# Optimization experiments

Measured on AMD Instinct MI355X. Metric: run time of the kernel, lower is better.

## Reference

```python
import jax, jax.numpy as jnp
import numpy as np

CH = 192; NH = 8; HD = CH // NH; WS = 8; OV = 2; WSO = WS + 2 * OV
SCALE = HD ** -0.5
B, H, W = 2, 256, 256

# static relative-position index (matches WindowMSA._idx)
_gy, _gx = np.meshgrid(np.arange(WS), np.arange(WS), indexing='ij')
_flat = np.stack([_gy.ravel(), _gx.ravel()])            # [2, ws*ws]
_rel = _flat[:, :, None] - _flat[:, None, :]
_rel[0] += WS - 1; _rel[1] += WS - 1; _rel[0] *= 2 * WS - 1
RPE_IDX = jnp.asarray(_rel.sum(0), dtype=jnp.int32)     # [64, 64]


def _ln(x, g, b, eps=1e-5):
    m = jnp.mean(x, -1, keepdims=True)
    v = jnp.mean((x - m) ** 2, -1, keepdims=True)
    return (x - m) * jax.lax.rsqrt(v + eps) * g + b


def _partition(xhw):  # [B,H,W,C] -> [B*nw, ws*ws, C]
    b, h, w, c = xhw.shape
    x = xhw.reshape(b, h // WS, WS, w // WS, WS, c).transpose(0, 1, 3, 2, 4, 5)
    return x.reshape(-1, WS * WS, c)


def _reverse(xw, h, w, b):  # [B*nw, ws*ws, C] -> [B,H,W,C]
    c = xw.shape[-1]
    x = xw.reshape(b, h // WS, w // WS, WS, WS, c).transpose(0, 1, 3, 2, 4, 5)
    return x.reshape(b, h, w, c)


def _mha(q, k, v, bias=None):  # q:[n,Nq,C] k,v:[n,Nk,C] split into heads
    n, nq, c = q.shape
    nk = k.shape[1]
    q = q.reshape(n, nq, NH, HD).transpose(0, 2, 1, 3)
    k = k.reshape(n, nk, NH, HD).transpose(0, 2, 1, 3)
    v = v.reshape(n, nk, NH, HD).transpose(0, 2, 1, 3)
    attn = jnp.einsum('bhnd,bhmd->bhnm', q, k) * SCALE
    if bias is not None:
        attn = attn + bias
    attn = jax.nn.softmax(attn, axis=-1)
    out = jnp.einsum('bhnm,bhmd->bhnd', attn, v)
    return out.transpose(0, 2, 1, 3).reshape(n, nq, c)


def _forward(x, g1, b1, qkv_w, rpe, wproj_w, g2, b2, mlp_w1, mlp_w2,
             alpha, og, ob, q_w, kv_w, oproj_w):
    b, c, h, w = x.shape  # H,W are multiples of WS -> no window padding
    xhw = x.transpose(0, 2, 3, 1)  # BHWC

    # --- window MSA branch (shift=False) ---
    xw = _partition(xhw)  # [b*nw, 64, C]
    xn = _ln(xw, g1, b1)
    qkv = xn @ qkv_w.T  # [n, 64, 3C]
    q, k, v = jnp.split(qkv, 3, axis=-1)
    bias = rpe[RPE_IDX].transpose(2, 0, 1)[None]  # [1, nh, 64, 64]
    msa = _mha(q, k, v, bias) @ wproj_w.T
    xw = xw + msa
    hmid = _ln(xw, g2, b2) @ mlp_w1.T
    xw = xw + jax.nn.gelu(hmid, approximate=False) @ mlp_w2.T
    x_win = _reverse(xw, h, w, b).transpose(0, 3, 1, 2)  # BCHW

    # --- overlapping cross attention branch ---
    xwin = _partition(xhw)  # queries from non-overlapped windows [n, 64, C]
    q = _ln(xwin, og, ob) @ q_w.T
    xp2 = jnp.pad(x, ((0, 0), (0, 0), (OV, OV), (OV, OV)), mode='reflect')
    xp2 = xp2.transpose(0, 2, 3, 1)  # [B, H+2ov, W+2ov, C]
    nh_w, nw_w = h // WS, w // WS
    rows = (jnp.arange(nh_w) * WS)[:, None] + jnp.arange(WSO)[None, :]
    cols = (jnp.arange(nw_w) * WS)[:, None] + jnp.arange(WSO)[None, :]
    xuf = xp2[:, rows]            # [B, nh_w, wso, W+2ov, C]
    xuf = xuf[:, :, :, cols]      # [B, nh_w, wso, nw_w, wso, C]
    xuf = xuf.transpose(0, 1, 3, 2, 4, 5).reshape(-1, WSO * WSO, c)
    kv = xuf @ kv_w.T             # [n, 144, 2C]
    k, v = jnp.split(kv, 2, axis=-1)
    out = _mha(q, k, v) @ oproj_w.T + xwin
    x_oca = _reverse(out, h, w, b).transpose(0, 3, 1, 2)

    return x + x_win * alpha + x_oca * (1.0 - alpha)


def setup_inputs():
    key = jax.random.key(0)
    ks = jax.random.split(key, 10)
    f = lambda k, shape: jax.random.normal(k, shape, jnp.float32) * 0.02
    return {
        'x': jax.random.normal(ks[0], (B, CH, H, W), jnp.float32),
        'g1': jnp.ones((CH,), jnp.float32), 'b1': jnp.zeros((CH,), jnp.float32),
        'qkv_w': f(ks[1], (3 * CH, CH)),
        'rpe': f(ks[2], ((2 * WS - 1) ** 2, NH)),
        'wproj_w': f(ks[3], (CH, CH)),
        'g2': jnp.ones((CH,), jnp.float32), 'b2': jnp.zeros((CH,), jnp.float32),
        'mlp_w1': f(ks[4], (2 * CH, CH)), 'mlp_w2': f(ks[5], (CH, 2 * CH)),
        'alpha': jnp.float32(0.5),
        'og': jnp.ones((CH,), jnp.float32), 'ob': jnp.zeros((CH,), jnp.float32),
        'q_w': f(ks[6], (CH, CH)), 'kv_w': f(ks[7], (2 * CH, CH)),
        'oproj_w': f(ks[8], (CH, CH)),
    }


def reference(x, g1, b1, qkv_w, rpe, wproj_w, g2, b2, mlp_w1, mlp_w2,
              alpha, og, ob, q_w, kv_w, oproj_w):
    return _forward(x, g1, b1, qkv_w, rpe, wproj_w, g2, b2, mlp_w1, mlp_w2,
                    alpha, og, ob, q_w, kv_w, oproj_w)
```

## Files before the change

kernel.cpp:

```cpp
#include <hip/hip_runtime.h>
#include <hip/hip_bf16.h>

typedef unsigned short u16;
typedef unsigned int   u32;
typedef __attribute__((ext_vector_type(8))) short bf16x8;
typedef __attribute__((ext_vector_type(4))) float f32x4;

#define CH   192
#define NH   8
#define HWD  256
#define LDW  200
#define QSTR 28
#define SCALE 0.20412414523193154f

__device__ __forceinline__ float bf2f(u16 u){ u32 v = ((u32)u) << 16; return __builtin_bit_cast(float, v); }
__device__ __forceinline__ u16 f2bf(float f){
  u32 u = __builtin_bit_cast(u32, f);
  u = (u + 0x7fffu + ((u >> 16) & 1u)) >> 16;
  return (u16)u;
}
__device__ __forceinline__ float lo2f(u32 p){ return __builtin_bit_cast(float, p << 16); }
__device__ __forceinline__ float hi2f(u32 p){ return __builtin_bit_cast(float, p & 0xffff0000u); }
__device__ __forceinline__ void up8(uint4 q, float* f){
  f[0]=lo2f(q.x); f[1]=hi2f(q.x); f[2]=lo2f(q.y); f[3]=hi2f(q.y);
// ... 61 lines not shown
  for (int e = 0; e < 8; ++e){
    float w = s[e];
    if (gv) w *= gv[kb + e];
    d[e] = f2bf(w);
  }
}
__global__ void k_cvec(const float* __restrict__ W, const float* __restrict__ g,
                       const float* __restrict__ b, float* __restrict__ c1,
                       float* __restrict__ c2, int K){
  int n = blockIdx.x; int l = threadIdx.x;
  float s1 = 0.f, s2 = 0.f;
  for (int k = l; k < K; k += 64){
    float w = W[(size_t)n*K + k];
    s1 += w*g[k]; s2 += w*b[k];
  }
  #pragma unroll
  for (int d = 1; d < 64; d <<= 1){ s1 += __shfl_xor(s1, d, 64); s2 += __shfl_xor(s2, d, 64); }
  if (l == 0){ c1[n] = s1; c2[n] = s2; }
}

__global__ __launch_bounds__(512) void k_kv(const float* __restrict__ x,
                                            const u16* __restrict__ wkv,
                                            u16* __restrict__ KV){
  __shared__ __align__(16) u16 sA[64*LDW];
  const int blk = blockIdx.x;
  const int batch = blk >> 10;
  const int pix0 = (blk & 1023) * 64;
  const float* xb = x + (size_t)batch*CH*65536;

  for (int idx = threadIdx.x; idx < 1536; idx += 512){
    int c = idx >> 3, s = idx & 7;
    const float* p = xb + (size_t)c*65536 + pix0 + s*8;
    float4 a = *reinterpret_cast<const float4*>(p);
    float4 b = *reinterpret_cast<const float4*>(p + 4);
    u16* d = &sA[(s*8)*LDW + c];
    d[0*LDW]=f2bf(a.x); d[1*LDW]=f2bf(a.y); d[2*LDW]=f2bf(a.z); d[3*LDW]=f2bf(a.w);
    d[4*LDW]=f2bf(b.x); d[5*LDW]=f2bf(b.y); d[6*LDW]=f2bf(b.z); d[7*LDW]=f2bf(b.w);
  }
  __syncthreads();

  const int w = threadIdx.x >> 6, l = threadIdx.x & 63;
  const int mt = w >> 1, half = w & 1;
  const f32x4 z4 = {0.f,0.f,0.f,0.f};
  f32x4 acc[12];
  #pragma unroll
  for (int j = 0; j < 12; ++j) acc[j] = z4;
  const int arow = mt*16 + (l & 15);
  for (int kt = 0; kt < 6; ++kt){
    bf16x8 a = afrag(sA, 0, LDW, arow, kt, l);
    #pragma unroll
    for (int j = 0; j < 12; ++j){
      int nt = half*12 + j;
      acc[j] = mfma16(a, bfrag(wkv, nt*6 + kt, l), acc[j]);
    }
  }
  u16* kvb = KV + ((size_t)batch*65536 + pix0)*384;
  const int rbase = mt*16 + ((l>>4)<<2);
  #pragma unroll
  for (int j = 0; j < 12; ++j){
    int col = (half*12 + j)*16 + (l & 15);
    #pragma unroll
    for (int r = 0; r < 4; ++r)
      kvb[(size_t)(rbase + r)*384 + col] = f2bf(acc[j][r]);
  }
}

#define P_   0
#define OW_  0
#define XO_  0
#define OQ_  12800
#define KF_  25600
#define VT_  30208
#define STM_ 35584
#define STS_ 35840
#define OST_ 36096
#define OPOOLN 36352

template<int MODE>
__global__ __launch_bounds__(512) void k_oca_attn(
    const float* __restrict__ x, const u16* __restrict__ ws16, const float* __restrict__ wsf,
    const float* __restrict__ alpha_p, float* __restrict__ out, u16* __restrict__ xoca)
{
  __shared__ __align__(16) u16 pool[OPOOLN];
  float* stm = reinterpret_cast<float*>(pool + STM_);
  float* sts = reinterpret_cast<float*>(pool + STS_);
  float* st  = reinterpret_cast<float*>(pool + OST_);
  const u16* KV = ws16 + WS_KV/2;
  const u16* WQ = ws16 + WS_WQ/2;
  const u16* WO = ws16 + WS_WO/2;
  const float* c1o = wsf + WS_C1O/4;
  const float* c2o = wsf + WS_C2O/4;

  const int tid = threadIdx.x;
  const int win = blockIdx.x;
  const int b  = win >> 10;
  const int wy = (win >> 5) & 31;
  const int wx = win & 31;
  const int hrow = wy*8, wcol = wx*8;
  const float* xb = x + (size_t)b*CH*HWD*HWD;
  float* outb = out + (size_t)b*CH*HWD*HWD;
  const size_t pixBase = (size_t)b*65536;
  const f32x4 z4 = {0.f,0.f,0.f,0.f};

  for (int j = tid; j < 1536; j += 512){
    int c = j >> 3, ty = j & 7;
    const float* src = xb + ((size_t)c*HWD + hrow + ty)*HWD + wcol;
    float4 a = *reinterpret_cast<const float4*>(src);
    float4 q = *reinterpret_cast<const float4*>(src + 4);
    u16* dst = &pool[OW_ + (ty*8)*LDW + c];
    dst[0*LDW]=f2bf(a.x); dst[1*LDW]=f2bf(a.y); dst[2*LDW]=f2bf(a.z); dst[3*LDW]=f2bf(a.w);
    dst[4*LDW]=f2bf(q.x); dst[5*LDW]=f2bf(q.y); dst[6*LDW]=f2bf(q.z); dst[7*LDW]=f2bf(q.w);
  }
  __syncthreads();
  ln_stats(pool + OW_, st, tid);
  __syncthreads();

  const int w = tid >> 6, l = tid & 63;
  const int mt = w >> 1;
  const int arow = mt*16 + (l & 15);
  const int rbase = mt*16 + ((l>>4)<<2);

  {
    const int half = w & 1;
    f32x4 acc[6];
    #pragma unroll
    for (int j = 0; j < 6; ++j) acc[j] = z4;
    for (int kt = 0; kt < 6; ++kt){
      bf16x8 a = afrag(pool, OW_, LDW, arow, kt, l);
      #pragma unroll
      for (int j = 0; j < 6; ++j)
        acc[j] = mfma16(a, bfrag(WQ, (half*6 + j)*6 + kt, l), acc[j]);
    }
    float mr[4], rr[4];
    #pragma unroll
    for (int r = 0; r < 4; ++r){ mr[r] = st[(rbase+r)*2]; rr[r] = st[(rbase+r)*2+1]; }
    #pragma unroll
    for (int j = 0; j < 6; ++j){
      int col = (half*6 + j)*16 + (l & 15);
      float c1v = c1o[col], c2v = c2o[col];
      #pragma unroll
      for (int r = 0; r < 4; ++r)
        pool[OQ_ + (rbase + r)*LDW + col] = f2bf(SCALE*(rr[r]*(acc[j][r] - mr[r]*c1v) + c2v));
    }
  }
  __syncthreads();

  {
    const uint4 zz = make_uint4(0,0,0,0);
    for (int i = tid; i < 64; i += 512)
      *reinterpret_cast<uint4*>(pool + OQ_ + i*LDW + 192) = zz;
    for (int i = tid; i < 144; i += 512)
      *reinterpret_cast<uint4*>(pool + KF_ + (i>>4)*512 + 384 + (i&15)*8) = zz;
    for (int i = tid; i < 672; i += 512)
      *reinterpret_cast<uint4*>(pool + VT_ + i*8) = zz;
    for (int i = tid; i < 128; i += 512)
      *reinterpret_cast<uint4*>(pool + P_ + (i>>1)*168 + 144 + (i&1)*8) = zz;
  }
  __syncthreads();

  const int ng   = w & 1;
  const int ntlo = ng ? 4 : 0;
  const int ntn  = ng ? 5 : 4;

  for (int h = 0; h < NH; ++h){
    for (int i = tid; i < 432; i += 512){
      int tok = i / 3, seg = i - tok*3;
      int ti = tok / 12, tj = tok - ti*12;
      int pix = refl(hrow + ti - 2)*HWD + refl(wcol + tj - 2);
      const u16* src = KV + (pixBase + (size_t)pix)*384 + h*24 + seg*8;
      uint4 kk = *reinterpret_cast<const uint4*>(src);
      uint4 vv = *reinterpret_cast<const uint4*>(src + 192);
      *reinterpret_cast<uint4*>(pool + KF_ + (tok>>4)*512 + (seg*16 + (tok&15))*8) = kk;
      const u16* vp = reinterpret_cast<const u16*>(&vv);
      #pragma unroll
      for (int e = 0; e < 8; ++e)
        pool[VT_ + (seg*8 + e)*168 + tok] = vp[e];
    }
    __syncthreads();

    f32x4 S[5];
    #pragma unroll
    for (int t = 0; t < 5; ++t) S[t] = z4;
    {
      bf16x8 a = *reinterpret_cast<const bf16x8*>(pool + OQ_ + arow*LDW + h*24 + ((l>>4)<<3));
      #pragma unroll
      for (int t = 0; t < 5; ++t)
        if (t < ntn)
          S[t] = mfma16(a, *reinterpret_cast<const bf16x8*>(pool + KF_ + (ntlo + t)*512 + l*8), z4);
    }
    #pragma unroll
    for (int r = 0; r < 4; ++r){
      float mx = -3.0e38f;
      #pragma unroll
      for (int t = 0; t < 5; ++t) if (t < ntn) mx = fmaxf(mx, S[t][r]);
      mx = fmaxf(mx, __shfl_xor(mx, 1, 64));
      mx = fmaxf(mx, __shfl_xor(mx, 2, 64));
      mx = fmaxf(mx, __shfl_xor(mx, 4, 64));
      mx = fmaxf(mx, __shfl_xor(mx, 8, 64));
      if ((l & 15) == 0) stm[(rbase + r)*2 + ng] = mx;
    }
    __syncthreads();

    #pragma unroll
    for (int r = 0; r < 4; ++r){
      int row = rbase + r;
      float m = fmaxf(stm[row*2], stm[row*2 + 1]);
      float sum = 0.f;
      #pragma unroll
      for (int t = 0; t < 5; ++t) if (t < ntn){
        float p = __expf(S[t][r] - m);
        sum += p;
        pool[P_ + row*168 + (ntlo + t)*16 + (l & 15)] = f2bf(p);
      }
      sum += __shfl_xor(sum, 1, 64);
      sum += __shfl_xor(sum, 2, 64);
      sum += __shfl_xor(sum, 4, 64);
      sum += __shfl_xor(sum, 8, 64);
      if ((l & 15) == 0) sts[row*2 + ng] = sum;
    }
    __syncthreads();

    {
      f32x4 O = z4;
      #pragma unroll
      for (int kt = 0; kt < 5; ++kt){
        bf16x8 pa = *reinterpret_cast<const bf16x8*>(pool + P_  + arow*168 + kt*32 + ((l>>4)<<3));
        bf16x8 vb = *reinterpret_cast<const bf16x8*>(pool + VT_ + (ng*16 + (l & 15))*168 + kt*32 + ((l>>4)<<3));
        O = mfma16(pa, vb, O);
      }
      int d = ng*16 + (l & 15);
      if (d < 24){
        #pragma unroll
        for (int r = 0; r < 4; ++r){
          int row = rbase + r;
          float inv = 1.f / (sts[row*2] + sts[row*2 + 1]);
          pool[OQ_ + row*LDW + h*24 + d] = f2bf(O[r]*inv);
        }
      }
    }
    __syncthreads();
  }

  {
    const int half = w & 1;
    f32x4 acc[6];
    #pragma unroll
    for (int j = 0; j < 6; ++j) acc[j] = z4;
    for (int kt = 0; kt < 6; ++kt){
      bf16x8 a = afrag(pool, OQ_, LDW, arow, kt, l);
      #pragma unroll
      for (int j = 0; j < 6; ++j)
        acc[j] = mfma16(a, bfrag(WO, (half*6 + j)*6 + kt, l), acc[j]);
    }
    __syncthreads();
    #pragma unroll
    for (int j = 0; j < 6; ++j){
      int col = (half*6 + j)*16 + (l & 15);
      #pragma unroll
      for (int r = 0; r < 4; ++r)
        pool[XO_ + (rbase + r)*LDW + col] = f2bf(acc[j][r]);
    }
  }
  __syncthreads();

  if (MODE == 0){
    float beta = 1.f - alpha_p[0];
    float xg = 1.f + beta;
    for (int j = tid; j < 1536; j += 512){
      int c = j >> 3, ty = j & 7;
      size_t goff = ((size_t)c*HWD + hrow + ty)*HWD + wcol;
      const float* src = xb + goff;
      float4 a = *reinterpret_cast<const float4*>(src);
      float4 q = *reinterpret_cast<const float4*>(src + 4);
      float wv[8];
      #pragma unroll
      for (int e = 0; e < 8; ++e) wv[e] = bf2f(pool[XO_ + (ty*8 + e)*LDW + c]);
      float4 o1 = make_float4(xg*a.x + beta*wv[0], xg*a.y + beta*wv[1], xg*a.z + beta*wv[2], xg*a.w + beta*wv[3]);
      float4 o2 = make_float4(xg*q.x + beta*wv[4], xg*q.y + beta*wv[5], xg*q.z + beta*wv[6], xg*q.w + beta*wv[7]);
      *reinterpret_cast<float4*>(outb + goff)     = o1;
      *reinterpret_cast<float4*>(outb + goff + 4) = o2;
    }
  } else {
    u16* xw = xoca + (size_t)win*12288;
    for (int j = tid; j < 1536; j += 512){
      int c = j >> 3, ty = j & 7;
      size_t goff = ((size_t)c*HWD + hrow + ty)*HWD + wcol;
      const float* src = xb + goff;
      float4 a = *reinterpret_cast<const float4*>(src);
      float4 q = *reinterpret_cast<const float4*>(src + 4);
      float xv[8] = {a.x,a.y,a.z,a.w,q.x,q.y,q.z,q.w};
      u32 wds[4];
      #pragma unroll
      for (int e = 0; e < 4; ++e){
        u32 lo = f2bf(bf2f(pool[XO_ + (ty*8 + 2*e  )*LDW + c]) + xv[2*e]);
        u32 hi = f2bf(bf2f(pool[XO_ + (ty*8 + 2*e+1)*LDW + c]) + xv[2*e+1]);
        wds[e] = lo | (hi << 16);
      }
      uint4 o; o.x = wds[0]; o.y = wds[1]; o.z = wds[2]; o.w = wds[3];
      *reinterpret_cast<uint4*>(xw + c*64 + ty*8) = o;
    }
  }
}

#define SX   0
#define SN   12800
#define SQKV 25600
#define SG   25600
#define SM   62464
#define SST  75264
#define POOLSZ 75520

template<int MODE>
__global__ __launch_bounds__(512) void k_msa(
    const float* __restrict__ x, const u16* __restrict__ ws16, const float* __restrict__ wsf,
    const float* __restrict__ rpe, const float* __restrict__ alpha_p, float* __restrict__ out,
    const u16* __restrict__ xoca)
{
  __shared__ __align__(16) u16 pool[POOLSZ];
  float* st = reinterpret_cast<float*>(pool + SST);
  const u16* W1  = ws16 + WS_W1/2;
  const u16* WP  = ws16 + WS_WP/2;
  const u16* WM1 = ws16 + WS_WM1/2;
  const u16* WM2 = ws16 + WS_WM2/2;
  const float* c1  = wsf + WS_C1/4;
  const float* c2  = wsf + WS_C2/4;
  const float* c1m = wsf + WS_C1M/4;
  const float* c2m = wsf + WS_C2M/4;

  const int tid = threadIdx.x;
  const int win = blockIdx.x;
  const int b  = win >> 10;
  const int wy = (win >> 5) & 31;
  const int wx = win & 31;
  const int hrow = wy*8, wcol = wx*8;
  const float* xb = x + (size_t)b*CH*HWD*HWD;
  float* outb = out + (size_t)b*CH*HWD*HWD;

  for (int j = tid; j < 1536; j += 512){
    int c = j >> 3, ty = j & 7;
    const float* src = xb + ((size_t)c*HWD + hrow + ty)*HWD + wcol;
    float4 a = *reinterpret_cast<const float4*>(src);
    float4 q = *reinterpret_cast<const float4*>(src + 4);
    u16* dst = &pool[SX + (ty*8)*LDW + c];
    dst[0*LDW]=f2bf(a.x); dst[1*LDW]=f2bf(a.y); dst[2*LDW]=f2bf(a.z); dst[3*LDW]=f2bf(a.w);
    dst[4*LDW]=f2bf(q.x); dst[5*LDW]=f2bf(q.y); dst[6*LDW]=f2bf(q.z); dst[7*LDW]=f2bf(q.w);
  }
  __syncthreads();
  ln_stats(pool + SX, st, tid);
  __syncthreads();

  const int w = tid >> 6, l = tid & 63;
  const int mt = w >> 1, half = w & 1;
  const int arow = mt*16 + (l & 15);
  const int rbase = mt*16 + ((l>>4)<<2);
  const f32x4 z4 = {0.f,0.f,0.f,0.f};

  {
    f32x4 acc[18];
    #pragma unroll
    for (int j = 0; j < 18; ++j) acc[j] = z4;
    for (int kt = 0; kt < 6; ++kt){
      bf16x8 a = afrag(pool, SX, LDW, arow, kt, l);
      #pragma unroll
      for (int j = 0; j < 18; ++j)
        acc[j] = mfma16(a, bfrag(W1, (half*18 + j)*6 + kt, l), acc[j]);
    }
    float mr[4], rr[4];
    #pragma unroll
    for (int r = 0; r < 4; ++r){ mr[r] = st[(rbase+r)*2]; rr[r] = st[(rbase+r)*2+1]; }
    #pragma unroll
    for (int j = 0; j < 18; ++j){
      int col = (half*18 + j)*16 + (l & 15);
      float c1v = c1[col], c2v = c2[col];
      #pragma unroll
      for (int r = 0; r < 4; ++r){
        int row = rbase + r;
        float v = rr[r]*(acc[j][r] - mr[r]*c1v) + c2v;
        pool[SQKV + row*576 + (col ^ (((row>>3)&7)<<3))] = f2bf(v);
      }
    }
  }
  __syncthreads();

  {
    const int t8 = tid >> 3, s8 = tid & 7;
    const int ry = t8 >> 3, rx = t8 & 7;
    const int swq = ((t8 >> 3) & 7) << 3;
    const int swk = s8 << 3;
    for (int h = 0; h < NH; ++h){
      float p[8];
      {
        float q24[24];
        #pragma unroll
        for (int seg = 0; seg < 3; ++seg){
          uint4 v = *reinterpret_cast<const uint4*>(pool + SQKV + t8*576 + ((h*24 + seg*8) ^ swq));
          up8(v, q24 + seg*8);
        }
        #pragma unroll
        for (int j = 0; j < 8; ++j){
          int c = s8*8 + j;
          float k24[24];
          #pragma unroll
          for (int seg = 0; seg < 3; ++seg){
            uint4 v = *reinterpret_cast<const uint4*>(pool + SQKV + c*576 + ((192 + h*24 + seg*8) ^ swk));
            up8(v, k24 + seg*8);
          }
          float s = 0.f;
          #pragma unroll
          for (int e = 0; e < 24; ++e) s += q24[e]*k24[e];
          int cy = c >> 3, cx = c & 7;
          p[j] = s*SCALE + rpe[((ry-cy+7)*15 + (rx-cx+7))*NH + h];
        }
      }
      float mx = p[0];
      #pragma unroll
      for (int j = 1; j < 8; ++j) mx = fmaxf(mx, p[j]);
      mx = fmaxf(mx, __shfl_xor(mx, 1, 64));
      mx = fmaxf(mx, __shfl_xor(mx, 2, 64));
      mx = fmaxf(mx, __shfl_xor(mx, 4, 64));
      float sum = 0.f;
      #pragma unroll
      for (int j = 0; j < 8; ++j){ p[j] = __expf(p[j] - mx); sum += p[j]; }
      sum += __shfl_xor(sum, 1, 64); sum += __shfl_xor(sum, 2, 64); sum += __shfl_xor(sum, 4, 64);
      float inv = 1.f / sum;
      float o24[24];
      #pragma unroll
      for (int seg = 0; seg < 3; ++seg){
        float o8[8];
        #pragma unroll
        for (int e = 0; e < 8; ++e) o8[e] = 0.f;
        #pragma unroll
        for (int j = 0; j < 8; ++j){
          int c = s8*8 + j;
          uint4 v = *reinterpret_cast<const uint4*>(pool + SQKV + c*576 + ((384 + h*24 + seg*8) ^ swk));
          float v8[8]; up8(v, v8);
          #pragma unroll
          for (int e = 0; e < 8; ++e) o8[e] += p[j]*v8[e];
        }
        #pragma unroll
        for (int e = 0; e < 8; ++e) o24[seg*8 + e] = o8[e];
      }
      #pragma unroll
      for (int e = 0; e < 24; ++e){
        o24[e] += __shfl_xor(o24[e], 1, 64);
        o24[e] += __shfl_xor(o24[e], 2, 64);
        o24[e] += __shfl_xor(o24[e], 4, 64);
      }
      u16* mrow = &pool[SM + t8*LDW + h*24 + s8*3];
      #pragma unroll
      for (int o = 0; o < 3; ++o) mrow[o] = f2bf(o24[s8*3 + o]*inv);
    }
  }
  __syncthreads();

  {
    f32x4 acc[6];
    #pragma unroll
    for (int j = 0; j < 6; ++j) acc[j] = z4;
    for (int kt = 0; kt < 6; ++kt){
      bf16x8 a = afrag(pool, SM, LDW, arow, kt, l);
      #pragma unroll
      for (int j = 0; j < 6; ++j)
        acc[j] = mfma16(a, bfrag(WP, (half*6 + j)*6 + kt, l), acc[j]);
    }
    #pragma unroll
    for (int j = 0; j < 6; ++j){
      int col = (half*6 + j)*16 + (l & 15);
      #pragma unroll
      for (int r = 0; r < 4; ++r){
        int row = rbase + r;
        pool[SN + row*LDW + col] = f2bf(acc[j][r] + bf2f(pool[SX + row*LDW + col]));
      }
    }
  }
  __syncthreads();
  ln_stats(pool + SN, st, tid);
  __syncthreads();

  {
    f32x4 acc[12];
    #pragma unroll
    for (int j = 0; j < 12; ++j) acc[j] = z4;
    for (int kt = 0; kt < 6; ++kt){
      bf16x8 a = afrag(pool, SN, LDW, arow, kt, l);
      #pragma unroll
      for (int j = 0; j < 12; ++j)
        acc[j] = mfma16(a, bfrag(WM1, (half*12 + j)*6 + kt, l), acc[j]);
    }
    float mr[4], rr[4];
    #pragma unroll
    for (int r = 0; r < 4; ++r){ mr[r] = st[(rbase+r)*2]; rr[r] = st[(rbase+r)*2+1]; }
    #pragma unroll
    for (int j = 0; j < 12; ++j){
      int col = (half*12 + j)*16 + (l & 15);
      float c1v = c1m[col], c2v = c2m[col];
      #pragma unroll
      for (int r = 0; r < 4; ++r){
        float hv = rr[r]*(acc[j][r] - mr[r]*c1v) + c2v;
        float gl = 0.5f*hv*(1.f + erff(hv*0.70710678118654752f));
        pool[SG + (rbase + r)*392 + col] = f2bf(gl);
      }
    }
  }
  __syncthreads();

  {
    f32x4 acc[6];
    #pragma unroll
    for (int j = 0; j < 6; ++j) acc[j] = z4;
    for (int kt = 0; kt < 12; ++kt){
      bf16x8 a = afrag(pool, SG, 392, arow, kt, l);
      #pragma unroll
      for (int j = 0; j < 6; ++j)
        acc[j] = mfma16(a, bfrag(WM2, (half*6 + j)*12 + kt, l), acc[j]);
    }
    #pragma unroll
    for (int j = 0; j < 6; ++j){
      int col = (half*6 + j)*16 + (l & 15);
      #pragma unroll
      for (int r = 0; r < 4; ++r){
        int row = rbase + r;
        pool[SM + row*LDW + col] = f2bf(acc[j][r] + bf2f(pool[SN + row*LDW + col]));
      }
    }
  }
  __syncthreads();

  float alpha = alpha_p[0];
  if (MODE == 0){
    for (int j = tid; j < 1536; j += 512){
      int c = j >> 3, ty = j & 7;
      size_t goff = ((size_t)c*HWD + hrow + ty)*HWD + wcol;
      float* dst = outb + goff;
      float4 a = *reinterpret_cast<const float4*>(dst);
      float4 q = *reinterpret_cast<const float4*>(dst + 4);
      float wv[8];
      #pragma unroll
      for (int e = 0; e < 8; ++e) wv[e] = bf2f(pool[SM + (ty*8 + e)*LDW + c]);
      float4 o1 = make_float4(a.x + alpha*wv[0], a.y + alpha*wv[1], a.z + alpha*wv[2], a.w + alpha*wv[3]);
      float4 o2 = make_float4(q.x + alpha*wv[4], q.y + alpha*wv[5], q.z + alpha*wv[6], q.w + alpha*wv[7]);
      *reinterpret_cast<float4*>(dst)     = o1;
      *reinterpret_cast<float4*>(dst + 4) = o2;
    }
  } else {
    float beta = 1.f - alpha;
    const u16* xw = xoca + (size_t)win*12288;
    for (int j = tid; j < 1536; j += 512){
      int c = j >> 3, ty = j & 7;
      size_t goff = ((size_t)c*HWD + hrow + ty)*HWD + wcol;
      const float* src = xb + goff;
      float4 a = *reinterpret_cast<const float4*>(src);
      float4 q = *reinterpret_cast<const float4*>(src + 4);
      uint4 oc = *reinterpret_cast<const uint4*>(xw + c*64 + ty*8);
      float ov[8]; up8(oc, ov);
      float wv[8];
      #pragma unroll
      for (int e = 0; e < 8; ++e) wv[e] = bf2f(pool[SM + (ty*8 + e)*LDW + c]);
      float4 o1 = make_float4(a.x + alpha*wv[0] + beta*ov[0], a.y + alpha*wv[1] + beta*ov[1],
                              a.z + alpha*wv[2] + beta*ov[2], a.w + alpha*wv[3] + beta*ov[3]);
      float4 o2 = make_float4(q.x + alpha*wv[4] + beta*ov[4], q.y + alpha*wv[5] + beta*ov[5],
                              q.z + alpha*wv[6] + beta*ov[6], q.w + alpha*wv[7] + beta*ov[7]);
      *reinterpret_cast<float4*>(outb + goff)     = o1;
      *reinterpret_cast<float4*>(outb + goff + 4) = o2;
    }
  }
}

__device__ __forceinline__ void layernorm_fb(const u16* __restrict__ src, u16* __restrict__ dst,
                                             const float* __restrict__ g, const float* __restrict__ b,
                                             int tid)
{
  int r = tid >> 3, sub = tid & 7;
  const u16* row = src + r*LDW + sub*24;
  float v[24];
  float s = 0.f, s2 = 0.f;
  #pragma unroll
  for (int e = 0; e < 24; ++e){ v[e] = bf2f(row[e]); s += v[e]; s2 += v[e]*v[e]; }
  s  += __shfl_xor(s, 1, 64);  s  += __shfl_xor(s, 2, 64);  s  += __shfl_xor(s, 4, 64);
  s2 += __shfl_xor(s2, 1, 64); s2 += __shfl_xor(s2, 2, 64); s2 += __shfl_xor(s2, 4, 64);
  float m   = s * (1.f/192.f);
  float var = s2 * (1.f/192.f) - m*m;
  float rs  = rsqrtf(var + 1e-5f);
  u16* drow = dst + r*LDW + sub*24;
  #pragma unroll
  for (int e = 0; e < 24; ++e)
    drow[e] = f2bf((v[e] - m) * rs * g[sub*24+e] + b[sub*24+e]);
}
__device__ __forceinline__ void gemm83(const u16* __restrict__ a_lds,
                                       const float* __restrict__ w0,
                                       const float* __restrict__ w1,
                                       const float* __restrict__ w2,
                                       int tg, float (*acc)[3])
{
  for (int k0 = 0; k0 < 192; k0 += 8){
    float wv[3][8];
    ldw8(w0 + k0, wv[0]); ldw8(w1 + k0, wv[1]); ldw8(w2 + k0, wv[2]);
    #pragma unroll
    for (int tt = 0; tt < 8; ++tt){
      float a[8];
      up8(*reinterpret_cast<const uint4*>(a_lds + (tg*8+tt)*LDW + k0), a);
      #pragma unroll
      for (int e = 0; e < 8; ++e){
        acc[tt][0] += a[e]*wv[0][e];
        acc[tt][1] += a[e]*wv[1][e];
        acc[tt][2] += a[e]*wv[2][e];
      }
    }
  }
}
__global__ __launch_bounds__(512) void k_msa_fb(
    const float* __restrict__ x, const float* __restrict__ g1, const float* __restrict__ b1,
    const float* __restrict__ qkv_w, const float* __restrict__ rpe, const float* __restrict__ wproj,
    const float* __restrict__ g2, const float* __restrict__ b2,
    const float* __restrict__ mlp1, const float* __restrict__ mlp2,
    const float* __restrict__ alpha_p, float* __restrict__ out)
{
  __shared__ __align__(16) u16 sX[64*LDW];
  __shared__ __align__(16) u16 sN[64*LDW];
  __shared__ __align__(16) u16 sM[64*LDW];
  __shared__ __align__(16) float sQ[64*QSTR];
  __shared__ __align__(16) float sK[64*QSTR];
  __shared__ __align__(16) float sV[64*QSTR];
  const int tid = threadIdx.x;
  const int win = blockIdx.x;
  const int b  = win >> 10;
  const int wy = (win >> 5) & 31;
  const int wx = win & 31;
  const int hrow = wy*8, wcol = wx*8;
  const float* xb = x + (size_t)b*CH*HWD*HWD;
  float* outb = out + (size_t)b*CH*HWD*HWD;
  for (int j = tid; j < 1536; j += 512){
    int c = j >> 3, ty = j & 7;
    const float* src = xb + ((size_t)c*HWD + hrow + ty)*HWD + wcol;
    float4 a = *reinterpret_cast<const float4*>(src);
    float4 q = *reinterpret_cast<const float4*>(src + 4);
    u16* dst = &sX[(ty*8)*LDW + c];
    dst[0*LDW]=f2bf(a.x); dst[1*LDW]=f2bf(a.y); dst[2*LDW]=f2bf(a.z); dst[3*LDW]=f2bf(a.w);
    dst[4*LDW]=f2bf(q.x); dst[5*LDW]=f2bf(q.y); dst[6*LDW]=f2bf(q.z); dst[7*LDW]=f2bf(q.w);
  }
  __syncthreads();
  layernorm_fb(sX, sN, g1, b1, tid);
  __syncthreads();
  const int t8 = tid >> 3, s8 = tid & 7;
  for (int h = 0; h < NH; ++h){
    {
      const u16* arow = &sN[t8*LDW];
      float acc[9];
      #pragma unroll
      for (int o = 0; o < 9; ++o) acc[o] = 0.f;
      const float* wp[9];
      #pragma unroll
      for (int o = 0; o < 3; ++o){
        const float* base = qkv_w + (size_t)(h*24 + s8*3 + o)*192;
        wp[o] = base; wp[3+o] = base + 192*192; wp[6+o] = base + 2*192*192;
      }
      for (int k0 = 0; k0 < 192; k0 += 8){
        float a[8]; up8(*reinterpret_cast<const uint4*>(arow + k0), a);
        #pragma unroll
        for (int o = 0; o < 9; ++o){
          float wv[8]; ldw8(wp[o] + k0, wv);
          #pragma unroll
          for (int e = 0; e < 8; ++e) acc[o] += a[e]*wv[e];
        }
      }
      #pragma unroll
      for (int o = 0; o < 3; ++o){
        sQ[t8*QSTR + s8*3 + o] = acc[o];
        sK[t8*QSTR + s8*3 + o] = acc[3+o];
        sV[t8*QSTR + s8*3 + o] = acc[6+o];
      }
    }
    __syncthreads();
    {
      float q24[24];
      #pragma unroll
      for (int e = 0; e < 24; ++e) q24[e] = sQ[t8*QSTR + e];
      const int ry = t8 >> 3, rx = t8 & 7;
      float p[8];
      #pragma unroll
      for (int j = 0; j < 8; ++j){
        int c = s8*8 + j;
        const float* kr = &sK[c*QSTR];
        float s = 0.f;
        #pragma unroll
        for (int e = 0; e < 24; ++e) s += q24[e]*kr[e];
        int cy = c >> 3, cx = c & 7;
        p[j] = s*SCALE + rpe[((ry-cy+7)*15 + (rx-cx+7))*NH + h];
      }
      float mx = p[0];
      #pragma unroll
      for (int j = 1; j < 8; ++j) mx = fmaxf(mx, p[j]);
      mx = fmaxf(mx, __shfl_xor(mx, 1, 64));
      mx = fmaxf(mx, __shfl_xor(mx, 2, 64));
      mx = fmaxf(mx, __shfl_xor(mx, 4, 64));
      float sum = 0.f;
      #pragma unroll
      for (int j = 0; j < 8; ++j){ p[j] = __expf(p[j] - mx); sum += p[j]; }
      sum += __shfl_xor(sum, 1, 64); sum += __shfl_xor(sum, 2, 64); sum += __shfl_xor(sum, 4, 64);
      float inv = 1.f / sum;
      float o24[24];
      #pragma unroll
      for (int e = 0; e < 24; ++e) o24[e] = 0.f;
      #pragma unroll
      for (int j = 0; j < 8; ++j){
        const float* vr = &sV[(s8*8 + j)*QSTR];
        #pragma unroll
        for (int e = 0; e < 24; ++e) o24[e] += p[j]*vr[e];
      }
      #pragma unroll
      for (int e = 0; e < 24; ++e){
        o24[e] += __shfl_xor(o24[e], 1, 64);
        o24[e] += __shfl_xor(o24[e], 2, 64);
        o24[e] += __shfl_xor(o24[e], 4, 64);
      }
      u16* mrow = &sM[t8*LDW + h*24 + s8*3];
      #pragma unroll
      for (int o = 0; o < 3; ++o) mrow[o] = f2bf(o24[s8*3 + o]*inv);
    }
    __syncthreads();
  }
  const int tg = tid >> 6, cg = tid & 63;
  {
    float acc[8][3];
    #pragma unroll
    for (int tt = 0; tt < 8; ++tt){ acc[tt][0]=0.f; acc[tt][1]=0.f; acc[tt][2]=0.f; }
    gemm83(sM, wproj + (size_t)(cg*3+0)*192, wproj + (size_t)(cg*3+1)*192, wproj + (size_t)(cg*3+2)*192, tg, acc);
    #pragma unroll
    for (int tt = 0; tt < 8; ++tt)
      #pragma unroll
      for (int j = 0; j < 3; ++j){
        int t = tg*8+tt, c = cg*3+j;
        sN[t*LDW + c] = f2bf(acc[tt][j] + bf2f(sX[t*LDW + c]));
      }
  }
  __syncthreads();
  layernorm_fb(sN, sX, g2, b2, tid);
  __syncthreads();
  float facc[8][3];
  #pragma unroll
  for (int tt = 0; tt < 8; ++tt){ facc[tt][0]=0.f; facc[tt][1]=0.f; facc[tt][2]=0.f; }
  for (int half = 0; half < 2; ++half){
    {
      float acc[8][3];
      #pragma unroll
      for (int tt = 0; tt < 8; ++tt){ acc[tt][0]=0.f; acc[tt][1]=0.f; acc[tt][2]=0.f; }
      gemm83(sX, mlp1 + (size_t)(half*192 + cg*3+0)*192, mlp1 + (size_t)(half*192 + cg*3+1)*192,
                 mlp1 + (size_t)(half*192 + cg*3+2)*192, tg, acc);
      #pragma unroll
      for (int tt = 0; tt < 8; ++tt)
        #pragma unroll
        for (int j = 0; j < 3; ++j){
          float vv = acc[tt][j];
          sM[(tg*8+tt)*LDW + cg*3+j] = f2bf(0.5f*vv*(1.f + erff(vv*0.70710678118654752f)));
        }
    }
    __syncthreads();
    gemm83(sM, mlp2 + (size_t)(cg*3+0)*384 + half*192, mlp2 + (size_t)(cg*3+1)*384 + half*192,
               mlp2 + (size_t)(cg*3+2)*384 + half*192, tg, facc);
    __syncthreads();
  }
  #pragma unroll
  for (int tt = 0; tt < 8; ++tt)
    #pragma unroll
    for (int j = 0; j < 3; ++j){
      int t = tg*8+tt, c = cg*3+j;
      sM[t*LDW + c] = f2bf(bf2f(sN[t*LDW + c]) + facc[tt][j]);
    }
  __syncthreads();
  float alpha = alpha_p[0];
  for (int j = tid; j < 1536; j += 512){
    int c = j >> 3, ty = j & 7;
    size_t goff = ((size_t)c*HWD + hrow + ty)*HWD + wcol;
    const float* src = xb + goff;
    float4 a = *reinterpret_cast<const float4*>(src);
    float4 q = *reinterpret_cast<const float4*>(src + 4);
    float wv[8];
    #pragma unroll
    for (int e = 0; e < 8; ++e) wv[e] = bf2f(sM[(ty*8 + e)*LDW + c]);
    float4 o1 = make_float4(a.x + alpha*wv[0], a.y + alpha*wv[1], a.z + alpha*wv[2], a.w + alpha*wv[3]);
    float4 o2 = make_float4(q.x + alpha*wv[4], q.y + alpha*wv[5], q.z + alpha*wv[6], q.w + alpha*wv[7]);
    *reinterpret_cast<float4*>(outb + goff)     = o1;
    *reinterpret_cast<float4*>(outb + goff + 4) = o2;
  }
}
__global__ __launch_bounds__(512) void k_oca_fb(
    const float* __restrict__ x, const float* __restrict__ og_p, const float* __restrict__ ob_p,
    const float* __restrict__ q_w, const float* __restrict__ kv_w, const float* __restrict__ oproj,
    const float* __restrict__ alpha_p, float* __restrict__ out)
{
  __shared__ __align__(16) u16 sW[64*LDW];
  __shared__ __align__(16) u16 sN[64*LDW];
  __shared__ __align__(16) u16 sQa[64*LDW];
  __shared__ __align__(16) u16 sU[144*LDW];
  __shared__ __align__(16) u16 sKb[144*32];
  __shared__ __align__(16) u16 sVb[144*32];
  const int tid = threadIdx.x;
  const int win = blockIdx.x;
  const int b  = win >> 10;
  const int wy = (win >> 5) & 31;
  const int wx = win & 31;
  const int hrow = wy*8, wcol = wx*8;
  const float* xb = x + (size_t)b*CH*HWD*HWD;
  float* outb = out + (size_t)b*CH*HWD*HWD;
  for (int j = tid; j < 1536; j += 512){
    int c = j >> 3, ty = j & 7;
    const float* src = xb + ((size_t)c*HWD + hrow + ty)*HWD + wcol;
    float4 a = *reinterpret_cast<const float4*>(src);
    float4 q = *reinterpret_cast<const float4*>(src + 4);
    u16* dst = &sW[(ty*8)*LDW + c];
    dst[0*LDW]=f2bf(a.x); dst[1*LDW]=f2bf(a.y); dst[2*LDW]=f2bf(a.z); dst[3*LDW]=f2bf(a.w);
    dst[4*LDW]=f2bf(q.x); dst[5*LDW]=f2bf(q.y); dst[6*LDW]=f2bf(q.z); dst[7*LDW]=f2bf(q.w);
  }
  for (int i = tid; i < 144*192; i += 512){
    int c = i / 144, t = i - c*144;
    int ti = t / 12, tj = t - ti*12;
    sU[t*LDW + c] = f2bf(xb[((size_t)c*HWD + refl(hrow + ti - 2))*HWD + refl(wcol + tj - 2)]);
  }
  __syncthreads();
  layernorm_fb(sW, sN, og_p, ob_p, tid);
  __syncthreads();
  const int tg = tid >> 6, cg = tid & 63;
  {
    float acc[8][3];
    #pragma unroll
    for (int tt = 0; tt < 8; ++tt){ acc[tt][0]=0.f; acc[tt][1]=0.f; acc[tt][2]=0.f; }
    gemm83(sN, q_w + (size_t)(cg*3+0)*192, q_w + (size_t)(cg*3+1)*192, q_w + (size_t)(cg*3+2)*192, tg, acc);
    #pragma unroll
    for (int tt = 0; tt < 8; ++tt)
      #pragma unroll
      for (int j = 0; j < 3; ++j)
        sQa[(tg*8+tt)*LDW + cg*3+j] = f2bf(acc[tt][j]);
  }
  __syncthreads();
  const int t8 = tid >> 3, s8 = tid & 7;
  for (int h = 0; h < NH; ++h){
    for (int i = tid; i < 144*24; i += 512){
      int tok = i / 24, d = i - tok*24;
      const float* kw = kv_w + (size_t)(h*24 + d)*192;
      const float* vw = kv_w + (size_t)(192 + h*24 + d)*192;
      const u16* arow = &sU[tok*LDW];
      float ka[4] = {0.f,0.f,0.f,0.f}, va[4] = {0.f,0.f,0.f,0.f};
      for (int k0 = 0; k0 < 192; k0 += 8){
        float a[8]; up8(*reinterpret_cast<const uint4*>(arow + k0), a);
        float kk[8]; ldw8(kw + k0, kk);
        float vv[8]; ldw8(vw + k0, vv);
        #pragma unroll
        for (int e = 0; e < 8; ++e){ ka[e&3] += a[e]*kk[e]; va[e&3] += a[e]*vv[e]; }
      }
      sKb[tok*32 + d] = f2bf(ka[0]+ka[1]+ka[2]+ka[3]);
      sVb[tok*32 + d] = f2bf(va[0]+va[1]+va[2]+va[3]);
    }
    __syncthreads();
    {
      float q24[24];
      #pragma unroll
      for (int e = 0; e < 24; ++e) q24[e] = bf2f(sQa[t8*LDW + h*24 + e]);
      float p[18];
      #pragma unroll
      for (int j = 0; j < 18; ++j){
        int c = s8*18 + j;
// ... 118 lines not shown
```

Measured before the change: 1.070 ms.

## Move window attention QK^T and PV onto MFMA with repacked shared layouts

Replaces the scalar per-thread dot-product attention in the window MSA kernel with 16x16 bf16 MFMA tiles for QK^T and P·V. Q is pre-scaled and K and V are written into zero-padded, fragment-friendly layouts (head dim padded from 24 to 32). Softmax uses cross-wave max and sum exchange through shared memory, with double-buffered probability tiles. The shared-memory plan is also reorganised to fit the new buffers. This adds several block-wide barriers per head and some padding waste in exchange for removing the heavy scalar FMA and shuffle work.

Measured after the change: 950.6 us. 11.2% less time.

```diff
diff --git a/kernel.cpp b/kernel.cpp
--- a/kernel.cpp
+++ b/kernel.cpp
@@ -387,13 +387,19 @@
   }
 }
 
-#define SX   0
-#define SN   12800
-#define SQKV 25600
-#define SG   25600
-#define SM   62464
-#define SST  75264
-#define POOLSZ 75520
+#define MSX  0
+#define MSQ  12800
+#define MKF  25600
+#define MVT  41984
+#define MP0  60416
+#define MP1  65024
+#define MSN  25600
+#define MXW  38400
+#define MSG  0
+#define MSTM 69632
+#define MSTS 70656
+#define MST  71168
+#define MPOOL 71424
 
 template<int MODE>
 __global__ __launch_bounds__(512) void k_msa(
@@ -401,8 +407,10 @@
     const float* __restrict__ rpe, const float* __restrict__ alpha_p, float* __restrict__ out,
     const u16* __restrict__ xoca)
 {
-  __shared__ __align__(16) u16 pool[POOLSZ];
-  float* st = reinterpret_cast<float*>(pool + SST);
+  __shared__ __align__(16) u16 pool[MPOOL];
+  float* stm = reinterpret_cast<float*>(pool + MSTM);
+  float* sts = reinterpret_cast<float*>(pool + MSTS);
+  float* st  = reinterpret_cast<float*>(pool + MST);
   const u16* W1  = ws16 + WS_W1/2;
   const u16* WP  = ws16 + WS_WP/2;
   const u16* WM1 = ws16 + WS_WM1/2;
@@ -420,32 +428,41 @@
   const int hrow = wy*8, wcol = wx*8;
   const float* xb = x + (size_t)b*CH*HWD*HWD;
   float* outb = out + (size_t)b*CH*HWD*HWD;
+  const f32x4 z4 = {0.f,0.f,0.f,0.f};
 
   for (int j = tid; j < 1536; j += 512){
     int c = j >> 3, ty = j & 7;
     const float* src = xb + ((size_t)c*HWD + hrow + ty)*HWD + wcol;
     float4 a = *reinterpret_cast<const float4*>(src);
     float4 q = *reinterpret_cast<const float4*>(src + 4);
-    u16* dst = &pool[SX + (ty*8)*LDW + c];
+    u16* dst = &pool[MSX + (ty*8)*LDW + c];
     dst[0*LDW]=f2bf(a.x); dst[1*LDW]=f2bf(a.y); dst[2*LDW]=f2bf(a.z); dst[3*LDW]=f2bf(a.w);
     dst[4*LDW]=f2bf(q.x); dst[5*LDW]=f2bf(q.y); dst[6*LDW]=f2bf(q.z); dst[7*LDW]=f2bf(q.w);
   }
-  __syncthreads();
-  ln_stats(pool + SX, st, tid);
+  {
+    const uint4 zz = make_uint4(0,0,0,0);
+    for (int i = tid; i < 2048; i += 512)
+      *reinterpret_cast<uint4*>(pool + MKF + i*8) = zz;
+    for (int i = tid; i < 2304; i += 512)
+      *reinterpret_cast<uint4*>(pool + MVT + i*8) = zz;
+    for (int i = tid; i < 64; i += 512)
+      *reinterpret_cast<uint4*>(pool + MSQ + i*LDW + 192) = zz;
+  }
+  __syncthreads();
+  ln_stats(pool + MSX, st, tid);
   __syncthreads();
 
   const int w = tid >> 6, l = tid & 63;
   const int mt = w >> 1, half = w & 1;
   const int arow = mt*16 + (l & 15);
   const int rbase = mt*16 + ((l>>4)<<2);
-  const f32x4 z4 = {0.f,0.f,0.f,0.f};
 
   {
     f32x4 acc[18];
     #pragma unroll
     for (int j = 0; j < 18; ++j) acc[j] = z4;
     for (int kt = 0; kt < 6; ++kt){
-      bf16x8 a = afrag(pool, SX, LDW, arow, kt, l);
+      bf16x8 a = afrag(pool, MSX, LDW, arow, kt, l);
       #pragma unroll
       for (int j = 0; j < 18; ++j)
         acc[j] = mfma16(a, bfrag(W1, (half*18 + j)*6 + kt, l), acc[j]);
@@ -455,111 +472,145 @@
     for (int r = 0; r < 4; ++r){ mr[r] = st[(rbase+r)*2]; rr[r] = st[(rbase+r)*2+1]; }
     #pragma unroll
     for (int j = 0; j < 18; ++j){
-      int col = (half*18 + j)*16 + (l & 15);
+      int tile = half*18 + j;
+      int col = tile*16 + (l & 15);
       float c1v = c1[col], c2v = c2[col];
+      if (tile < 12){
+        #pragma unroll
+        for (int r = 0; r < 4; ++r){
+          int row = rbase + r;
+          float v = rr[r]*(acc[j][r] - mr[r]*c1v) + c2v;
+          pool[MSQ + row*LDW + col] = f2bf(SCALE*v);
+        }
+      } else if (tile < 24){
+        int d = col - 192; int h = d/24; int dd = d - h*24;
+        int base = MKF + h*2048 + ((((dd>>3)<<4))<<3) + (dd&7);
+        #pragma unroll
+        for (int r = 0; r < 4; ++r){
+          int row = rbase + r;
+          float v = rr[r]*(acc[j][r] - mr[r]*c1v) + c2v;
+          pool[base + ((row>>4)<<9) + ((row&15)<<3)] = f2bf(v);
+        }
+      } else {
+        int d = col - 384; int h = d/24; int dd = d - h*24;
+        int base = MVT + h*2304 + dd*72;
+        #pragma unroll
+        for (int r = 0; r < 4; ++r){
+          int row = rbase + r;
+          float v = rr[r]*(acc[j][r] - mr[r]*c1v) + c2v;
+          pool[base + row] = f2bf(v);
+        }
+      }
+    }
+  }
+  __syncthreads();
+
+  {
+    const int ng = half;
+    int bidx[2][4];
+    #pragma unroll
+    for (int t = 0; t < 2; ++t)
+      #pragma unroll
+      for (int r = 0; r < 4; ++r){
+        int row = rbase + r, col = (ng*2 + t)*16 + (l & 15);
+        bidx[t][r] = (((row>>3)-(col>>3)+7)*15 + ((row&7)-(col&7)+7))*NH;
+      }
+    for (int hg = 0; hg < 2; ++hg){
+      f32x4 S[4][2];
+      #pragma unroll
+      for (int hh = 0; hh < 4; ++hh){
+        int h = hg*4 + hh;
+        bf16x8 a = *reinterpret_cast<const bf16x8*>(pool + MSQ + arow*LDW + h*24 + ((l>>4)<<3));
+        #pragma unroll
+        for (int t = 0; t < 2; ++t)
+          S[hh][t] = mfma16(a, *reinterpret_cast<const bf16x8*>(pool + MKF + h*2048 + (ng*2+t)*512 + l*8), z4);
+      }
+      #pragma unroll
+      for (int hh = 0; hh < 4; ++hh){
+        int h = hg*4 + hh;
+        #pragma unroll
+        for (int t = 0; t < 2; ++t)
+          #pragma unroll
+          for (int r = 0; r < 4; ++r)
+            S[hh][t][r] += rpe[bidx[t][r] + h];
+        #pragma unroll
+        for (int r = 0; r < 4; ++r){
+          float mx = fmaxf(S[hh][0][r], S[hh][1][r]);
+          mx = fmaxf(mx, __shfl_xor(mx, 1, 64));
+          mx = fmaxf(mx, __shfl_xor(mx, 2, 64));
+          mx = fmaxf(mx, __shfl_xor(mx, 4, 64));
+          mx = fmaxf(mx, __shfl_xor(mx, 8, 64));
+          if ((l & 15) == 0) stm[hh*128 + (rbase+r)*2 + ng] = mx;
+        }
+      }
+      __syncthreads();
+      #pragma unroll
+      for (int hh = 0; hh < 4; ++hh){
+        int h = hg*4 + hh;
+        u16* Pb = pool + ((h & 1) ? MP1 : MP0);
+        float* sb = sts + (h & 1)*128;
+        #pragma unroll
+        for (int r = 0; r < 4; ++r){
+          int row = rbase + r;
+          float m = fmaxf(stm[hh*128 + row*2], stm[hh*128 + row*2 + 1]);
+          float sum = 0.f;
+          #pragma unroll
+          for (int t = 0; t < 2; ++t){
+            float p = __expf(S[hh][t][r] - m);
+            sum += p;
+            Pb[row*72 + (ng*2+t)*16 + (l & 15)] = f2bf(p);
+          }
+          sum += __shfl_xor(sum, 1, 64);
+          sum += __shfl_xor(sum, 2, 64);
+          sum += __shfl_xor(sum, 4, 64);
+          sum += __shfl_xor(sum, 8, 64);
+          if ((l & 15) == 0) sb[row*2 + ng] = sum;
+        }
+        __syncthreads();
+        f32x4 O = z4;
+        #pragma unroll
+        for (int kt = 0; kt < 2; ++kt){
+          bf16x8 pa = *reinterpret_cast<const bf16x8*>(Pb + arow*72 + kt*32 + ((l>>4)<<3));
+          bf16x8 vb = *reinterpret_cast<const bf16x8*>(pool + MVT + h*2304 + (ng*16 + (l & 15))*72 + kt*32 + ((l>>4)<<3));
+          O = mfma16(pa, vb, O);
+        }
+        int d = ng*16 + (l & 15);
+        if (d < 24){
+          #pragma unroll
+          for (int r = 0; r < 4; ++r){
+            int row = rbase + r;
+            float inv = 1.f / (sb[row*2] + sb[row*2 + 1]);
+            pool[MSQ + row*LDW + h*24 + d] = f2bf(O[r]*inv);
+          }
+        }
+      }
+    }
+  }
+  __syncthreads();
+
+  {
+    f32x4 acc[6];
+    #pragma unroll
+    for (int j = 0; j < 6; ++j) acc[j] = z4;
+    for (int kt = 0; kt < 6; ++kt){
+      bf16x8 a = afrag(pool, MSQ, LDW, arow, kt, l);
+      #pragma unroll
+      for (int j = 0; j < 6; ++j)
+        acc[j] = mfma16(a, bfrag(WP, (half*6 + j)*6 + kt, l), acc[j]);
+    }
+    __syncthreads();
+    #pragma unroll
+    for (int j = 0; j < 6; ++j){
+      int col = (half*6 + j)*16 + (l & 15);
       #pragma unroll
       for (int r = 0; r < 4; ++r){
         int row = rbase + r;
-        float v = rr[r]*(acc[j][r] - mr[r]*c1v) + c2v;
-        pool[SQKV + row*576 + (col ^ (((row>>3)&7)<<3))] = f2bf(v);
-      }
-    }
-  }
-  __syncthreads();
-
-  {
-    const int t8 = tid >> 3, s8 = tid & 7;
-    const int ry = t8 >> 3, rx = t8 & 7;
-    const int swq = ((t8 >> 3) & 7) << 3;
-    const int swk = s8 << 3;
-    for (int h = 0; h < NH; ++h){
-      float p[8];
-      {
-        float q24[24];
-        #pragma unroll
-        for (int seg = 0; seg < 3; ++seg){
-          uint4 v = *reinterpret_cast<const uint4*>(pool + SQKV + t8*576 + ((h*24 + seg*8) ^ swq));
-          up8(v, q24 + seg*8);
-        }
-        #pragma unroll
-        for (int j = 0; j < 8; ++j){
-          int c = s8*8 + j;
-          float k24[24];
-          #pragma unroll
-          for (int seg = 0; seg < 3; ++seg){
-            uint4 v = *reinterpret_cast<const uint4*>(pool + SQKV + c*576 + ((192 + h*24 + seg*8) ^ swk));
-            up8(v, k24 + seg*8);
-          }
-          float s = 0.f;
-          #pragma unroll
-          for (int e = 0; e < 24; ++e) s += q24[e]*k24[e];
-          int cy = c >> 3, cx = c & 7;
-          p[j] = s*SCALE + rpe[((ry-cy+7)*15 + (rx-cx+7))*NH + h];
-        }
-      }
-      float mx = p[0];
-      #pragma unroll
-      for (int j = 1; j < 8; ++j) mx = fmaxf(mx, p[j]);
-      mx = fmaxf(mx, __shfl_xor(mx, 1, 64));
-      mx = fmaxf(mx, __shfl_xor(mx, 2, 64));
-      mx = fmaxf(mx, __shfl_xor(mx, 4, 64));
-      float sum = 0.f;
-      #pragma unroll
-      for (int j = 0; j < 8; ++j){ p[j] = __expf(p[j] - mx); sum += p[j]; }
-      sum += __shfl_xor(sum, 1, 64); sum += __shfl_xor(sum, 2, 64); sum += __shfl_xor(sum, 4, 64);
-      float inv = 1.f / sum;
-      float o24[24];
-      #pragma unroll
-      for (int seg = 0; seg < 3; ++seg){
-        float o8[8];
-        #pragma unroll
-        for (int e = 0; e < 8; ++e) o8[e] = 0.f;
-        #pragma unroll
-        for (int j = 0; j < 8; ++j){
-          int c = s8*8 + j;
-          uint4 v = *reinterpret_cast<const uint4*>(pool + SQKV + c*576 + ((384 + h*24 + seg*8) ^ swk));
-          float v8[8]; up8(v, v8);
-          #pragma unroll
-          for (int e = 0; e < 8; ++e) o8[e] += p[j]*v8[e];
-        }
-        #pragma unroll
-        for (int e = 0; e < 8; ++e) o24[seg*8 + e] = o8[e];
-      }
-      #pragma unroll
-      for (int e = 0; e < 24; ++e){
-        o24[e] += __shfl_xor(o24[e], 1, 64);
-        o24[e] += __shfl_xor(o24[e], 2, 64);
-        o24[e] += __shfl_xor(o24[e], 4, 64);
-      }
-      u16* mrow = &pool[SM + t8*LDW + h*24 + s8*3];
-      #pragma unroll
-      for (int o = 0; o < 3; ++o) mrow[o] = f2bf(o24[s8*3 + o]*inv);
-    }
-  }
-  __syncthreads();
-
-  {
-    f32x4 acc[6];
-    #pragma unroll
-    for (int j = 0; j < 6; ++j) acc[j] = z4;
-    for (int kt = 0; kt < 6; ++kt){
-      bf16x8 a = afrag(pool, SM, LDW, arow, kt, l);
-      #pragma unroll
-      for (int j = 0; j < 6; ++j)
-        acc[j] = mfma16(a, bfrag(WP, (half*6 + j)*6 + kt, l), acc[j]);
-    }
-    #pragma unroll
-    for (int j = 0; j < 6; ++j){
-      int col = (half*6 + j)*16 + (l & 15);
-      #pragma unroll
-      for (int r = 0; r < 4; ++r){
-        int row = rbase + r;
-        pool[SN + row*LDW + col] = f2bf(acc[j][r] + bf2f(pool[SX + row*LDW + col]));
-      }
-    }
-  }
-  __syncthreads();
-  ln_stats(pool + SN, st, tid);
+        pool[MSN + row*LDW + col] = f2bf(acc[j][r] + bf2f(pool[MSX + row*LDW + col]));
+      }
+    }
+  }
+  __syncthreads();
+  ln_stats(pool + MSN, st, tid);
   __syncthreads();
 
   {
@@ -567,7 +618,7 @@
     #pragma unroll
     for (int j = 0; j < 12; ++j) acc[j] = z4;
     for (int kt = 0; kt < 6; ++kt){
-      bf16x8 a = afrag(pool, SN, LDW, arow, kt, l);
+      bf16x8 a = afrag(pool, MSN, LDW, arow, kt, l);
       #pragma unroll
       for (int j = 0; j < 12; ++j)
         acc[j] = mfma16(a, bfrag(WM1, (half*12 + j)*6 + kt, l), acc[j]);
@@ -575,6 +626,7 @@
     float mr[4], rr[4];
     #pragma unroll
     for (int r = 0; r < 4; ++r){ mr[r] = st[(rbase+r)*2]; rr[r] = st[(rbase+r)*2+1]; }
+    __syncthreads();
     #pragma unroll
     for (int j = 0; j < 12; ++j){
       int col = (half*12 + j)*16 + (l & 15);
@@ -583,7 +635,7 @@
       for (int r = 0; r < 4; ++r){
         float hv = rr[r]*(acc[j][r] - mr[r]*c1v) + c2v;
         float gl = 0.5f*hv*(1.f + erff(hv*0.70710678118654752f));
-        pool[SG + (rbase + r)*392 + col] = f2bf(gl);
+        pool[MSG + (rbase + r)*392 + col] = f2bf(gl);
       }
     }
   }
@@ -594,7 +646,7 @@
     #pragma unroll
     for (int j = 0; j < 6; ++j) acc[j] = z4;
     for (int kt = 0; kt < 12; ++kt){
-      bf16x8 a = afrag(pool, SG, 392, arow, kt, l);
+      bf16x8 a = afrag(pool, MSG, 392, arow, kt, l);
       #pragma unroll
       for (int j = 0; j < 6; ++j)
         acc[j] = mfma16(a, bfrag(WM2, (half*6 + j)*12 + kt, l), acc[j]);
@@ -605,7 +657,7 @@
       #pragma unroll
       for (int r = 0; r < 4; ++r){
         int row = rbase + r;
-        pool[SM + row*LDW + col] = f2bf(acc[j][r] + bf2f(pool[SN + row*LDW + col]));
+        pool[MXW + row*LDW + col] = f2bf(acc[j][r] + bf2f(pool[MSN + row*LDW + col]));
       }
     }
   }
@@ -621,7 +673,7 @@
       float4 q = *reinterpret_cast<const float4*>(dst + 4);
       float wv[8];
       #pragma unroll
-      for (int e = 0; e < 8; ++e) wv[e] = bf2f(pool[SM + (ty*8 + e)*LDW + c]);
+      for (int e = 0; e < 8; ++e) wv[e] = bf2f(pool[MXW + (ty*8 + e)*LDW + c]);
       float4 o1 = make_float4(a.x + alpha*wv[0], a.y + alpha*wv[1], a.z + alpha*wv[2], a.w + alpha*wv[3]);
       float4 o2 = make_float4(q.x + alpha*wv[4], q.y + alpha*wv[5], q.z + alpha*wv[6], q.w + alpha*wv[7]);
       *reinterpret_cast<float4*>(dst)     = o1;
@@ -640,7 +692,7 @@
       float ov[8]; up8(oc, ov);
       float wv[8];
       #pragma unroll
-      for (int e = 0; e < 8; ++e) wv[e] = bf2f(pool[SM + (ty*8 + e)*LDW + c]);
+      for (int e = 0; e < 8; ++e) wv[e] = bf2f(pool[MXW + (ty*8 + e)*LDW + c]);
       float4 o1 = make_float4(a.x + alpha*wv[0] + beta*ov[0], a.y + alpha*wv[1] + beta*ov[1],
                               a.z + alpha*wv[2] + beta*ov[2], a.w + alpha*wv[3] + beta*ov[3]);
       float4 o2 = make_float4(q.x + alpha*wv[4] + beta*ov[4], q.y + alpha*wv[5] + beta*ov[5],
```
